# Kernel tuning notes

Hardware: AMD Instinct MI355X
Metric: run time of the kernel (lower is better)

The kernel has to match this reference:

```python
import jax, jax.numpy as jnp
import numpy as np

D_MODEL = 128
D_HIDDEN = 256
D_STATE = 16
EXPAND = 2
D_INNER = EXPAND * D_MODEL  # 256
DT_RANK = (D_MODEL + 15) // 16  # 8, mamba_ssm default ceil(d_model/16)
N = 8192  # decoded reads (sequence length for Mamba)
M = 8192  # encoded reads


def setup_inputs() -> dict:
    key = jax.random.key(0)
    ks = jax.random.split(key, 16)
    s = 0.02
    return {
        "encoded_reads": jax.random.normal(ks[0], (M, D_MODEL), jnp.float32),
        "decoded_reads": jax.random.normal(ks[1], (N, D_MODEL), jnp.float32),
        # Mamba block params (d_conv=1 -> depthwise conv is per-channel affine)
        "in_proj_w": jax.random.normal(ks[2], (2 * D_INNER, D_MODEL), jnp.float32) * s,
        "conv_w": jax.random.normal(ks[3], (D_INNER,), jnp.float32) * s + 1.0,
        "conv_b": jnp.zeros((D_INNER,), jnp.float32),
        "x_proj_w": jax.random.normal(ks[4], (DT_RANK + 2 * D_STATE, D_INNER), jnp.float32) * s,
        "dt_proj_w": jax.random.normal(ks[5], (D_INNER, DT_RANK), jnp.float32) * s,
        "dt_proj_b": jnp.full((D_INNER,), -4.0, jnp.float32),  # softplus(-4)~0.018, typical dt init
        "A_log": jnp.log(jnp.broadcast_to(jnp.arange(1, D_STATE + 1, dtype=jnp.float32), (D_INNER, D_STATE))),
        "D": jnp.ones((D_INNER,), jnp.float32),
        "out_proj_w": jax.random.normal(ks[6], (D_MODEL, D_INNER), jnp.float32) * s,
        # query/key projections (nn.Linear with bias)
        "q_w": jax.random.normal(ks[7], (D_HIDDEN, D_MODEL), jnp.float32) * s,
        "q_b": jnp.zeros((D_HIDDEN,), jnp.float32),
        "k_w": jax.random.normal(ks[8], (D_HIDDEN, D_MODEL), jnp.float32) * s,
        "k_b": jnp.zeros((D_HIDDEN,), jnp.float32),
    }


def _mamba(u, in_proj_w, conv_w, conv_b, x_proj_w, dt_proj_w, dt_proj_b, A_log, D, out_proj_w):
    # u: [L, d_model] treated as a single sequence
    xz = u @ in_proj_w.T                         # [L, 2*d_inner]
    x, z = jnp.split(xz, 2, axis=-1)             # [L, d_inner] each
    # depthwise conv1d with kernel size 1 == per-channel affine, then SiLU
    x = jax.nn.silu(x * conv_w + conv_b)
    x_dbl = x @ x_proj_w.T                       # [L, dt_rank + 2*d_state]
    dt, B, C = jnp.split(x_dbl, [DT_RANK, DT_RANK + D_STATE], axis=-1)
    dt = jax.nn.softplus(dt @ dt_proj_w.T + dt_proj_b)  # [L, d_inner]
    A = -jnp.exp(A_log)                          # [d_inner, d_state]
    deltaA = jnp.exp(dt[:, :, None] * A)         # [L, d_inner, d_state]
    deltaBx = dt[:, :, None] * B[:, None, :] * x[:, :, None]  # [L, d_inner, d_state]

    def step(h, inp):
        dA_t, dBx_t, C_t = inp
        h = dA_t * h + dBx_t                     # [d_inner, d_state]
        y_t = jnp.einsum('dn,n->d', h, C_t)      # [d_inner]
        return h, y_t

    h0 = jnp.zeros((D_INNER, D_STATE), x.dtype)
    _, y = jax.lax.scan(step, h0, (deltaA, deltaBx, C))  # y: [L, d_inner]
    y = (y + D * x) * jax.nn.silu(z)
    return y @ out_proj_w.T                      # [L, d_model]


def reference(encoded_reads, decoded_reads, in_proj_w, conv_w, conv_b, x_proj_w,
              dt_proj_w, dt_proj_b, A_log, D, out_proj_w, q_w, q_b, k_w, k_b):
    decoded_processed = _mamba(decoded_reads, in_proj_w, conv_w, conv_b, x_proj_w,
                               dt_proj_w, dt_proj_b, A_log, D, out_proj_w)
    queries = decoded_processed @ q_w.T + q_b    # [N, d_hidden]
    keys = encoded_reads @ k_w.T + k_b           # [M, d_hidden]
    scores = jnp.einsum('nd,md->nm', queries, keys)
    return jax.nn.softmax(scores, axis=-1)
```

## Files before the change

### kernel.cpp

```cpp
#include <hip/hip_runtime.h>
#include <hip/hip_bf16.h>

typedef __attribute__((ext_vector_type(8))) short bf16x8;
typedef __attribute__((ext_vector_type(4))) float f32x4;

#define LSEQ 8192
#define CHUNK 64
#define NCHUNK 128

__device__ __forceinline__ void gload16(const void* g, void* l) {
    __builtin_amdgcn_global_load_lds(
        (const __attribute__((address_space(1))) void*)g,
        (__attribute__((address_space(3))) void*)l,
        16, 0, 0);
}

__global__ void cvt_bf16_k(const float* __restrict__ src, __hip_bfloat16* __restrict__ dst, int n) {
    int i = blockIdx.x * blockDim.x + threadIdx.x;
    if (i < n) dst[i] = __float2bfloat16(src[i]);
}

template<int OUT_BF16, int HAS_BIAS>
__global__ __launch_bounds__(256) void gemm_bt_k(
    const __hip_bfloat16* __restrict__ A,
    const __hip_bfloat16* __restrict__ B,
    float* __restrict__ Cf, __hip_bfloat16* __restrict__ Cb,
    const float* __restrict__ bias, int M, int N, int K)
{
    __shared__ __hip_bfloat16 As[64][32];
    __shared__ __hip_bfloat16 Bs[64][32];
    const int tid  = threadIdx.x;
    const int wave = tid >> 6;
    const int lane = tid & 63;
    const int wm = (wave >> 1) << 5;
    const int wn = (wave & 1) << 5;
    const long bm = (long)blockIdx.y << 6;
    const long bn = (long)blockIdx.x << 6;

    f32x4 acc[2][2] = {{{0.f,0.f,0.f,0.f},{0.f,0.f,0.f,0.f}},
                       {{0.f,0.f,0.f,0.f},{0.f,0.f,0.f,0.f}}};

    const int sr = tid >> 2;
    const int sc = (tid & 3) << 3;
    const int lr = lane & 15;
    const int kg = (lane >> 4) << 3;

    for (int k0 = 0; k0 < K; k0 += 32) {
        {
            long ar = bm + sr;
            bf16x8 av = {0,0,0,0,0,0,0,0};
            if (ar < M) av = *(const bf16x8*)(A + ar * K + k0 + sc);
            *(bf16x8*)&As[sr][sc] = av;
            long br = bn + sr;
            bf16x8 bv = {0,0,0,0,0,0,0,0};
            if (br < N) bv = *(const bf16x8*)(B + br * K + k0 + sc);
            *(bf16x8*)&Bs[sr][sc] = bv;
        }
        __syncthreads();
        bf16x8 a0 = *(const bf16x8*)&As[wm + lr][kg];
        bf16x8 a1 = *(const bf16x8*)&As[wm + 16 + lr][kg];
        bf16x8 b0 = *(const bf16x8*)&Bs[wn + lr][kg];
        bf16x8 b1 = *(const bf16x8*)&Bs[wn + 16 + lr][kg];
        acc[0][0] = __builtin_amdgcn_mfma_f32_16x16x32_bf16(a0, b0, acc[0][0], 0, 0, 0);
        acc[0][1] = __builtin_amdgcn_mfma_f32_16x16x32_bf16(a0, b1, acc[0][1], 0, 0, 0);
        acc[1][0] = __builtin_amdgcn_mfma_f32_16x16x32_bf16(a1, b0, acc[1][0], 0, 0, 0);
        acc[1][1] = __builtin_amdgcn_mfma_f32_16x16x32_bf16(a1, b1, acc[1][1], 0, 0, 0);
        __syncthreads();
    }
    const int rg = (lane >> 4) << 2;
    #pragma unroll
    for (int i = 0; i < 2; ++i)
      #pragma unroll
      for (int j = 0; j < 2; ++j)
        #pragma unroll
        for (int r = 0; r < 4; ++r) {
            long row = bm + wm + i * 16 + rg + r;
            long col = bn + wn + j * 16 + lr;
            if (row < M && col < N) {
                float v = acc[i][j][r];
                if (HAS_BIAS) v += bias[col];
                if (OUT_BF16) Cb[row * N + col] = __float2bfloat16(v);
                else          Cf[row * N + col] = v;
            }
        }
}

template<int PASS>
__global__ __launch_bounds__(256) void scores_k(
    const __hip_bfloat16* __restrict__ Q, const __hip_bfloat16* __restrict__ Kb,
    float* __restrict__ out, const float* __restrict__ invZ)
{
    __shared__ alignas(16) char Asb[128 * 128];
    __shared__ alignas(16) char Bsb[128 * 128];
    const int tid = threadIdx.x, wave = tid >> 6, lane = tid & 63;
    const int bm = blockIdx.y << 7, bn = blockIdx.x << 7;
    const int wm = (wave >> 1) << 6, wn = (wave & 1) << 6;
    const int K = 256;

    f32x4 acc[4][4];
    #pragma unroll
    for (int i = 0; i < 4; ++i)
      #pragma unroll
      for (int j = 0; j < 4; ++j)
        acc[i][j] = (f32x4){0.f, 0.f, 0.f, 0.f};

    for (int k0 = 0; k0 < 256; k0 += 64) {
        #pragma unroll
        for (int c = 0; c < 4; ++c) {
            const int base = (wave * 4 + c) * 1024;
            const int o = base + lane * 16;
            const int q = o ^ (((o >> 7) & 7) << 4);
            const int row = q >> 7, col = (q & 127) >> 1;
            gload16(Q  + (size_t)(bm + row) * K + k0 + col, Asb + base);
            gload16(Kb + (size_t)(bn + row) * K + k0 + col, Bsb + base);
        }
        __syncthreads();
        #pragma unroll
        for (int ks = 0; ks < 2; ++ks) {
            bf16x8 af[4], bfr[4];
            const int cb = ks * 64 + ((lane >> 4) << 4);
            #pragma unroll
            for (int i = 0; i < 4; ++i) {
                const int ra = wm + i * 16 + (lane & 15);
                af[i]  = *(const bf16x8*)(Asb + ((ra * 128 + cb) ^ ((ra & 7) << 4)));
                const int rb = wn + i * 16 + (lane & 15);
                bfr[i] = *(const bf16x8*)(Bsb + ((rb * 128 + cb) ^ ((rb & 7) << 4)));
            }
            #pragma unroll
            for (int i = 0; i < 4; ++i)
              #pragma unroll
              for (int j = 0; j < 4; ++j)
                acc[i][j] = __builtin_amdgcn_mfma_f32_16x16x32_bf16(af[i], bfr[j], acc[i][j], 0, 0, 0);
        }
        __syncthreads();
    }

    const int lr = lane & 15, rg = (lane >> 4) << 2;
    if (PASS == 0) {
        #pragma unroll
        for (int i = 0; i < 4; ++i) {
            #pragma unroll
            for (int r = 0; r < 4; ++r) {
                float s = __expf(acc[i][0][r]) + __expf(acc[i][1][r])
                        + __expf(acc[i][2][r]) + __expf(acc[i][3][r]);
                #pragma unroll
                for (int o = 1; o < 16; o <<= 1) s += __shfl_xor(s, o, 64);
                if (lr == 0)
                    out[(size_t)(blockIdx.x * 2 + (wave & 1)) * 8192
                        + bm + wm + i * 16 + rg + r] = s;
            }
        }
    } else {
        #pragma unroll
        for (int i = 0; i < 4; ++i)
          #pragma unroll
          for (int r = 0; r < 4; ++r) {
            const int row = bm + wm + i * 16 + rg + r;
            const float iz = invZ[row];
            #pragma unroll
            for (int j = 0; j < 4; ++j)
                out[(size_t)row * 8192 + bn + wn + j * 16 + lr] = __expf(acc[i][j][r]) * iz;
          }
    }
}

__global__ __launch_bounds__(256) void rowsum_inv_k(
    const float* __restrict__ partial, float* __restrict__ invZ)
{
    const int row = blockIdx.x * 256 + threadIdx.x;
    float s = 0.0f;
    for (int c = 0; c < 128; ++c) s += partial[(size_t)c * 8192 + row];
    invZ[row] = 1.0f / s;
}

__global__ __launch_bounds__(256) void conv_silu_k(
    const float* __restrict__ xz, const float* __restrict__ cw, const float* __restrict__ cb,
    float* __restrict__ xf, __hip_bfloat16* __restrict__ xb, float* __restrict__ zs)
{
    const int t = blockIdx.x, d = threadIdx.x;
    float xv = xz[(size_t)t * 512 + d] * cw[d] + cb[d];
    xv = xv / (1.0f + __expf(-xv));
    float zv = xz[(size_t)t * 512 + 256 + d];
    zv = zv / (1.0f + __expf(-zv));
    xf[(size_t)t * 256 + d] = xv;
    xb[(size_t)t * 256 + d] = __float2bfloat16(xv);
    zs[(size_t)t * 256 + d] = zv;
}

__global__ __launch_bounds__(256) void dt_k(
    const float* __restrict__ xdbl, const float* __restrict__ dtw,
    const float* __restrict__ dtb, float* __restrict__ dtv)
{
    __shared__ float r8[8];
    const int t = blockIdx.x, d = threadIdx.x;
    if (d < 8) r8[d] = xdbl[(size_t)t * 40 + d];
    __syncthreads();
    float acc = dtb[d];
    #pragma unroll
    for (int r = 0; r < 8; ++r) acc += r8[r] * dtw[d * 8 + r];
    float sp = (acc > 20.0f) ? acc : logf(1.0f + expf(acc));
    dtv[(size_t)t * 256 + d] = sp;
}

__global__ __launch_bounds__(256) void scan_chunk_k(
    const float* __restrict__ dtv, const float* __restrict__ xf,
    const float* __restrict__ xdbl, const float* __restrict__ A_log,
    float* __restrict__ P, float* __restrict__ S)
{
    __shared__ float Bl[CHUNK * 16];
    const int c = blockIdx.x, d = threadIdx.x;
    const int t0 = c * CHUNK;
    for (int k = d; k < CHUNK * 16; k += 256) {
        int tt = k >> 4, n = k & 15;
        Bl[k] = xdbl[(size_t)(t0 + tt) * 40 + 8 + n];
    }
    __syncthreads();
    float An[16], Pv[16], Sv[16];
    #pragma unroll
    for (int n = 0; n < 16; ++n) { An[n] = -expf(A_log[d * 16 + n]); Pv[n] = 1.0f; Sv[n] = 0.0f; }
    for (int tt = 0; tt < CHUNK; ++tt) {
        float dt = dtv[(size_t)(t0 + tt) * 256 + d];
        float xv = xf[(size_t)(t0 + tt) * 256 + d];
        float dtx = dt * xv;
        #pragma unroll
        for (int n = 0; n < 16; ++n) {
            float a = __expf(dt * An[n]);
            Pv[n] *= a;
            Sv[n] = a * Sv[n] + dtx * Bl[tt * 16 + n];
        }
    }
    size_t base = (size_t)c * 4096 + (size_t)d * 16;
    #pragma unroll
    for (int n = 0; n < 16; ++n) { P[base + n] = Pv[n]; S[base + n] = Sv[n]; }
}

__global__ __launch_bounds__(256) void scan_carry_k(
    const float* __restrict__ P, const float* __restrict__ S, float* __restrict__ hinit)
{
    const int ch = blockIdx.x * 256 + threadIdx.x;
    float h = 0.0f;
    for (int c = 0; c < NCHUNK; ++c) {
        hinit[(size_t)c * 4096 + ch] = h;
        h = P[(size_t)c * 4096 + ch] * h + S[(size_t)c * 4096 + ch];
    }
}

__global__ __launch_bounds__(256) void scan_final_k(
    const float* __restrict__ dtv, const float* __restrict__ xf,
    const float* __restrict__ xdbl, const float* __restrict__ A_log,
    const float* __restrict__ hinit, const float* __restrict__ Dp,
    const float* __restrict__ zs, __hip_bfloat16* __restrict__ yfb)
{
    __shared__ float Bl[CHUNK * 16];
    __shared__ float Cl[CHUNK * 16];
    const int c = blockIdx.x, d = threadIdx.x;
    const int t0 = c * CHUNK;
    for (int k = d; k < CHUNK * 16; k += 256) {
        int tt = k >> 4, n = k & 15;
        Bl[k] = xdbl[(size_t)(t0 + tt) * 40 + 8 + n];
        Cl[k] = xdbl[(size_t)(t0 + tt) * 40 + 24 + n];
    }
    __syncthreads();
    float An[16], h[16];
    #pragma unroll
    for (int n = 0; n < 16; ++n) {
        An[n] = -expf(A_log[d * 16 + n]);
        h[n] = hinit[(size_t)c * 4096 + (size_t)d * 16 + n];
    }
    const float Dv = Dp[d];
    for (int tt = 0; tt < CHUNK; ++tt) {
        float dt = dtv[(size_t)(t0 + tt) * 256 + d];
        float xv = xf[(size_t)(t0 + tt) * 256 + d];
        float dtx = dt * xv;
        float y = 0.0f;
        #pragma unroll
        for (int n = 0; n < 16; ++n) {
            float a = __expf(dt * An[n]);
            h[n] = a * h[n] + dtx * Bl[tt * 16 + n];
            y += h[n] * Cl[tt * 16 + n];
        }
        float outv = (y + Dv * xv) * zs[(size_t)(t0 + tt) * 256 + d];
        yfb[(size_t)(t0 + tt) * 256 + d] = __float2bfloat16(outv);
    }
}

__global__ __launch_bounds__(256) void wc_k(
    const float* __restrict__ qw, const float* __restrict__ opw, __hip_bfloat16* __restrict__ wcb)
{
    const int hh = blockIdx.x, d = threadIdx.x;
    float acc = 0.0f;
    for (int m = 0; m < 128; ++m) acc += qw[hh * 128 + m] * opw[m * 256 + d];
    wcb[hh * 256 + d] = __float2bfloat16(acc);
}

extern "C" void kernel_launch(void* const* d_in, const int* in_sizes, int n_in,
                              void* d_out, int out_size, void* d_ws, size_t ws_size,
                              hipStream_t stream)
{
    const float* enc        = (const float*)d_in[0];
    const float* dec        = (const float*)d_in[1];
    const float* in_proj_w  = (const float*)d_in[2];
    const float* conv_w     = (const float*)d_in[3];
    const float* conv_b     = (const float*)d_in[4];
    const float* x_proj_w   = (const float*)d_in[5];
    const float* dt_proj_w  = (const float*)d_in[6];
    const float* dt_proj_b  = (const float*)d_in[7];
    const float* A_log      = (const float*)d_in[8];
    const float* Dp         = (const float*)d_in[9];
    const float* out_proj_w = (const float*)d_in[10];
    const float* q_w        = (const float*)d_in[11];
    const float* q_b        = (const float*)d_in[12];
    const float* k_w        = (const float*)d_in[13];
    const float* k_b        = (const float*)d_in[14];

    char* ws = (char*)d_ws;
    size_t off = 0;
    auto alloc = [&](size_t bytes) -> void* {
        void* p = ws + off;
        off += (bytes + 255) & ~(size_t)255;
        return p;
    };
    __hip_bfloat16* ub   = (__hip_bfloat16*)alloc((size_t)8192 * 128 * 2);
    __hip_bfloat16* encb = (__hip_bfloat16*)alloc((size_t)8192 * 128 * 2);
    __hip_bfloat16* wib  = (__hip_bfloat16*)alloc((size_t)512 * 128 * 2);
    __hip_bfloat16* wxb  = (__hip_bfloat16*)alloc((size_t)40 * 256 * 2);
    __hip_bfloat16* kwb  = (__hip_bfloat16*)alloc((size_t)256 * 128 * 2);
    __hip_bfloat16* wcb  = (__hip_bfloat16*)alloc((size_t)256 * 256 * 2);
    float* xz    = (float*)alloc((size_t)8192 * 512 * 4);
    float* xf    = (float*)alloc((size_t)8192 * 256 * 4);
    __hip_bfloat16* xb = (__hip_bfloat16*)alloc((size_t)8192 * 256 * 2);
    float* zs    = (float*)alloc((size_t)8192 * 256 * 4);
    float* xdbl  = (float*)alloc((size_t)8192 * 40 * 4);
    float* dtv   = (float*)alloc((size_t)8192 * 256 * 4);
    float* P     = (float*)alloc((size_t)NCHUNK * 4096 * 4);
    float* Ssum  = (float*)alloc((size_t)NCHUNK * 4096 * 4);
    float* hinit = (float*)alloc((size_t)NCHUNK * 4096 * 4);
    __hip_bfloat16* yfb = (__hip_bfloat16*)alloc((size_t)8192 * 256 * 2);
    __hip_bfloat16* qbm = (__hip_bfloat16*)alloc((size_t)8192 * 256 * 2);
    __hip_bfloat16* kbm = (__hip_bfloat16*)alloc((size_t)8192 * 256 * 2);
    float* partial = (float*)alloc((size_t)128 * 8192 * 4);
    float* invZ    = (float*)alloc((size_t)8192 * 4);
    (void)ws_size;

    cvt_bf16_k<<<(8192 * 128 + 255) / 256, 256, 0, stream>>>(dec, ub, 8192 * 128);
    cvt_bf16_k<<<(8192 * 128 + 255) / 256, 256, 0, stream>>>(enc, encb, 8192 * 128);
    cvt_bf16_k<<<(512 * 128 + 255) / 256, 256, 0, stream>>>(in_proj_w, wib, 512 * 128);
    cvt_bf16_k<<<(40 * 256 + 255) / 256, 256, 0, stream>>>(x_proj_w, wxb, 40 * 256);
    cvt_bf16_k<<<(256 * 128 + 255) / 256, 256, 0, stream>>>(k_w, kwb, 256 * 128);

    {
        dim3 g(512 / 64, 8192 / 64);
        gemm_bt_k<0, 0><<<g, 256, 0, stream>>>(ub, wib, xz, nullptr, nullptr, 8192, 512, 128);
    }
    conv_silu_k<<<8192, 256, 0, stream>>>(xz, conv_w, conv_b, xf, xb, zs);

    {
        dim3 g(1, 8192 / 64);
        gemm_bt_k<0, 0><<<g, 256, 0, stream>>>(xb, wxb, xdbl, nullptr, nullptr, 8192, 40, 256);
    }
    dt_k<<<8192, 256, 0, stream>>>(xdbl, dt_proj_w, dt_proj_b, dtv);

    scan_chunk_k<<<NCHUNK, 256, 0, stream>>>(dtv, xf, xdbl, A_log, P, Ssum);
    scan_carry_k<<<16, 256, 0, stream>>>(P, Ssum, hinit);
    scan_final_k<<<NCHUNK, 256, 0, stream>>>(dtv, xf, xdbl, A_log, hinit, Dp, zs, yfb);

    wc_k<<<256, 256, 0, stream>>>(q_w, out_proj_w, wcb);

    {
        dim3 g(256 / 64, 8192 / 64);
        gemm_bt_k<1, 1><<<g, 256, 0, stream>>>(yfb, wcb, nullptr, qbm, q_b, 8192, 256, 256);
    }
    {
        dim3 g(256 / 64, 8192 / 64);
        gemm_bt_k<1, 1><<<g, 256, 0, stream>>>(encb, kwb, nullptr, kbm, k_b, 8192, 256, 128);
    }

    {
        dim3 g(8192 / 128, 8192 / 128);
        scores_k<0><<<g, 256, 0, stream>>>(qbm, kbm, partial, nullptr);
        rowsum_inv_k<<<8192 / 256, 256, 0, stream>>>(partial, invZ);
        scores_k<1><<<g, 256, 0, stream>>>(qbm, kbm, (float*)d_out, invZ);
    }
}
```

Baseline: 287.7 us.

## Fuse conversions, conv/SiLU and dt projection into GEMMs and scan kernels

Merges all weight conversions and the out_proj·q_w weight fold into one prep kernel, and makes the in_proj and key GEMMs read fp32 activations directly, converting them to bf16 while loading into LDS. The conv+SiLU epilogue moves into the in_proj GEMM, and the dt projection with its softplus is recomputed inside both scan kernels from xdbl kept in LDS. The scan chunk size is halved to 32 so twice as many blocks run, and the LDS rows are padded to 40 to reduce bank conflicts. This removes several launches and the xz, dtv and bf16 input round-trips through memory, at the cost of computing softplus twice and a longer carry-scan loop.

```diff
diff --git a/kernel.cpp b/kernel.cpp
--- a/kernel.cpp
+++ b/kernel.cpp
@@ -4,9 +4,8 @@
 typedef __attribute__((ext_vector_type(8))) short bf16x8;
 typedef __attribute__((ext_vector_type(4))) float f32x4;
 
-#define LSEQ 8192
-#define CHUNK 64
-#define NCHUNK 128
+#define CHUNK 32
+#define NCHUNK 256
 
 __device__ __forceinline__ void gload16(const void* g, void* l) {
     __builtin_amdgcn_global_load_lds(
@@ -15,9 +14,27 @@
         16, 0, 0);
 }
 
-__global__ void cvt_bf16_k(const float* __restrict__ src, __hip_bfloat16* __restrict__ dst, int n) {
-    int i = blockIdx.x * blockDim.x + threadIdx.x;
-    if (i < n) dst[i] = __float2bfloat16(src[i]);
+__device__ __forceinline__ float silu_f(float v) { return v / (1.0f + __expf(-v)); }
+
+__global__ __launch_bounds__(256) void prep_k(
+    const float* __restrict__ in_proj_w, const float* __restrict__ x_proj_w,
+    const float* __restrict__ k_w, const float* __restrict__ q_w,
+    const float* __restrict__ out_proj_w,
+    __hip_bfloat16* __restrict__ wib, __hip_bfloat16* __restrict__ wxb,
+    __hip_bfloat16* __restrict__ kwb, __hip_bfloat16* __restrict__ wcb)
+{
+    const int b = blockIdx.x, t = threadIdx.x;
+    if (b < 424) {
+        int idx = b * 256 + t;
+        if (idx < 65536)      wib[idx]         = __float2bfloat16(in_proj_w[idx]);
+        else if (idx < 75776) wxb[idx - 65536] = __float2bfloat16(x_proj_w[idx - 65536]);
+        else                  kwb[idx - 75776] = __float2bfloat16(k_w[idx - 75776]);
+    } else {
+        const int hh = b - 424;
+        float acc = 0.0f;
+        for (int m = 0; m < 128; ++m) acc += q_w[hh * 128 + m] * out_proj_w[m * 256 + t];
+        wcb[hh * 256 + t] = __float2bfloat16(acc);
+    }
 }
 
 template<int OUT_BF16, int HAS_BIAS>
@@ -27,8 +44,8 @@
     float* __restrict__ Cf, __hip_bfloat16* __restrict__ Cb,
     const float* __restrict__ bias, int M, int N, int K)
 {
-    __shared__ __hip_bfloat16 As[64][32];
-    __shared__ __hip_bfloat16 Bs[64][32];
+    __shared__ __hip_bfloat16 As[64][40];
+    __shared__ __hip_bfloat16 Bs[64][40];
     const int tid  = threadIdx.x;
     const int wave = tid >> 6;
     const int lane = tid & 63;
@@ -81,6 +98,83 @@
                 if (HAS_BIAS) v += bias[col];
                 if (OUT_BF16) Cb[row * N + col] = __float2bfloat16(v);
                 else          Cf[row * N + col] = v;
+            }
+        }
+}
+
+template<int EPI>
+__global__ __launch_bounds__(256) void gemm_f32a_k(
+    const float* __restrict__ A, const __hip_bfloat16* __restrict__ B,
+    const float* __restrict__ w0, const float* __restrict__ w1,
+    float* __restrict__ xf, __hip_bfloat16* __restrict__ ob, float* __restrict__ zs,
+    int M, int N, int K)
+{
+    __shared__ __hip_bfloat16 As[64][40];
+    __shared__ __hip_bfloat16 Bs[64][40];
+    const int tid  = threadIdx.x;
+    const int wave = tid >> 6;
+    const int lane = tid & 63;
+    const int wm = (wave >> 1) << 5;
+    const int wn = (wave & 1) << 5;
+    const long bm = (long)blockIdx.y << 6;
+    const long bn = (long)blockIdx.x << 6;
+
+    f32x4 acc[2][2] = {{{0.f,0.f,0.f,0.f},{0.f,0.f,0.f,0.f}},
+                       {{0.f,0.f,0.f,0.f},{0.f,0.f,0.f,0.f}}};
+
+    const int sr = tid >> 2;
+    const int sc = (tid & 3) << 3;
+    const int lr = lane & 15;
+    const int kg = (lane >> 4) << 3;
+
+    for (int k0 = 0; k0 < K; k0 += 32) {
+        {
+            long ar = bm + sr;
+            f32x4 x0 = *(const f32x4*)(A + ar * K + k0 + sc);
+            f32x4 x1 = *(const f32x4*)(A + ar * K + k0 + sc + 4);
+            union { bf16x8 v; __hip_bfloat16 h[8]; } u;
+            u.h[0] = __float2bfloat16(x0[0]); u.h[1] = __float2bfloat16(x0[1]);
+            u.h[2] = __float2bfloat16(x0[2]); u.h[3] = __float2bfloat16(x0[3]);
+            u.h[4] = __float2bfloat16(x1[0]); u.h[5] = __float2bfloat16(x1[1]);
+            u.h[6] = __float2bfloat16(x1[2]); u.h[7] = __float2bfloat16(x1[3]);
+            *(bf16x8*)&As[sr][sc] = u.v;
+            long br = bn + sr;
+            bf16x8 bv = {0,0,0,0,0,0,0,0};
+            if (br < N) bv = *(const bf16x8*)(B + br * K + k0 + sc);
+            *(bf16x8*)&Bs[sr][sc] = bv;
+        }
+        __syncthreads();
+        bf16x8 a0 = *(const bf16x8*)&As[wm + lr][kg];
+        bf16x8 a1 = *(const bf16x8*)&As[wm + 16 + lr][kg];
+        bf16x8 b0 = *(const bf16x8*)&Bs[wn + lr][kg];
+        bf16x8 b1 = *(const bf16x8*)&Bs[wn + 16 + lr][kg];
+        acc[0][0] = __builtin_amdgcn_mfma_f32_16x16x32_bf16(a0, b0, acc[0][0], 0, 0, 0);
+        acc[0][1] = __builtin_amdgcn_mfma_f32_16x16x32_bf16(a0, b1, acc[0][1], 0, 0, 0);
+        acc[1][0] = __builtin_amdgcn_mfma_f32_16x16x32_bf16(a1, b0, acc[1][0], 0, 0, 0);
+        acc[1][1] = __builtin_amdgcn_mfma_f32_16x16x32_bf16(a1, b1, acc[1][1], 0, 0, 0);
+        __syncthreads();
+    }
+    const int rg = (lane >> 4) << 2;
+    #pragma unroll
+    for (int i = 0; i < 2; ++i)
+      #pragma unroll
+      for (int j = 0; j < 2; ++j)
+        #pragma unroll
+        for (int r = 0; r < 4; ++r) {
+            long row = bm + wm + i * 16 + rg + r;
+            long col = bn + wn + j * 16 + lr;
+            float v = acc[i][j][r];
+            if (EPI == 0) {
+                if (col < 256) {
+                    float xv = v * w0[col] + w1[col];
+                    float s = silu_f(xv);
+                    xf[row * 256 + col] = s;
+                    ob[row * 256 + col] = __float2bfloat16(s);
+                } else {
+                    zs[row * 256 + col - 256] = silu_f(v);
+                }
+            } else {
+                ob[row * N + col] = __float2bfloat16(v + w0[col]);
             }
         }
 }
@@ -173,60 +267,35 @@
     invZ[row] = 1.0f / s;
 }
 
-__global__ __launch_bounds__(256) void conv_silu_k(
-    const float* __restrict__ xz, const float* __restrict__ cw, const float* __restrict__ cb,
-    float* __restrict__ xf, __hip_bfloat16* __restrict__ xb, float* __restrict__ zs)
-{
-    const int t = blockIdx.x, d = threadIdx.x;
-    float xv = xz[(size_t)t * 512 + d] * cw[d] + cb[d];
-    xv = xv / (1.0f + __expf(-xv));
-    float zv = xz[(size_t)t * 512 + 256 + d];
-    zv = zv / (1.0f + __expf(-zv));
-    xf[(size_t)t * 256 + d] = xv;
-    xb[(size_t)t * 256 + d] = __float2bfloat16(xv);
-    zs[(size_t)t * 256 + d] = zv;
-}
-
-__global__ __launch_bounds__(256) void dt_k(
-    const float* __restrict__ xdbl, const float* __restrict__ dtw,
-    const float* __restrict__ dtb, float* __restrict__ dtv)
-{
-    __shared__ float r8[8];
-    const int t = blockIdx.x, d = threadIdx.x;
-    if (d < 8) r8[d] = xdbl[(size_t)t * 40 + d];
-    __syncthreads();
-    float acc = dtb[d];
-    #pragma unroll
-    for (int r = 0; r < 8; ++r) acc += r8[r] * dtw[d * 8 + r];
-    float sp = (acc > 20.0f) ? acc : logf(1.0f + expf(acc));
-    dtv[(size_t)t * 256 + d] = sp;
-}
-
 __global__ __launch_bounds__(256) void scan_chunk_k(
-    const float* __restrict__ dtv, const float* __restrict__ xf,
-    const float* __restrict__ xdbl, const float* __restrict__ A_log,
+    const float* __restrict__ xf, const float* __restrict__ xdbl,
+    const float* __restrict__ dtw, const float* __restrict__ dtb,
+    const float* __restrict__ A_log,
     float* __restrict__ P, float* __restrict__ S)
 {
-    __shared__ float Bl[CHUNK * 16];
+    __shared__ float xs[CHUNK * 40];
     const int c = blockIdx.x, d = threadIdx.x;
     const int t0 = c * CHUNK;
-    for (int k = d; k < CHUNK * 16; k += 256) {
-        int tt = k >> 4, n = k & 15;
-        Bl[k] = xdbl[(size_t)(t0 + tt) * 40 + 8 + n];
-    }
+    for (int k = d; k < CHUNK * 40; k += 256) xs[k] = xdbl[(size_t)t0 * 40 + k];
     __syncthreads();
+    const f32x4 wa = *(const f32x4*)(dtw + d * 8);
+    const f32x4 wb = *(const f32x4*)(dtw + d * 8 + 4);
+    const float dbias = dtb[d];
     float An[16], Pv[16], Sv[16];
     #pragma unroll
     for (int n = 0; n < 16; ++n) { An[n] = -expf(A_log[d * 16 + n]); Pv[n] = 1.0f; Sv[n] = 0.0f; }
     for (int tt = 0; tt < CHUNK; ++tt) {
-        float dt = dtv[(size_t)(t0 + tt) * 256 + d];
+        const float* xr = xs + tt * 40;
+        float dr = dbias + xr[0]*wa[0] + xr[1]*wa[1] + xr[2]*wa[2] + xr[3]*wa[3]
+                         + xr[4]*wb[0] + xr[5]*wb[1] + xr[6]*wb[2] + xr[7]*wb[3];
+        float dt = (dr > 20.0f) ? dr : logf(1.0f + expf(dr));
         float xv = xf[(size_t)(t0 + tt) * 256 + d];
         float dtx = dt * xv;
         #pragma unroll
         for (int n = 0; n < 16; ++n) {
             float a = __expf(dt * An[n]);
             Pv[n] *= a;
-            Sv[n] = a * Sv[n] + dtx * Bl[tt * 16 + n];
+            Sv[n] = a * Sv[n] + dtx * xr[8 + n];
         }
     }
     size_t base = (size_t)c * 4096 + (size_t)d * 16;
@@ -246,21 +315,20 @@
 }
 
 __global__ __launch_bounds__(256) void scan_final_k(
-    const float* __restrict__ dtv, const float* __restrict__ xf,
-    const float* __restrict__ xdbl, const float* __restrict__ A_log,
-    const float* __restrict__ hinit, const float* __restrict__ Dp,
-    const float* __restrict__ zs, __hip_bfloat16* __restrict__ yfb)
-{
-    __shared__ float Bl[CHUNK * 16];
-    __shared__ float Cl[CHUNK * 16];
+    const float* __restrict__ xf, const float* __restrict__ xdbl,
+    const float* __restrict__ dtw, const float* __restrict__ dtb,
+    const float* __restrict__ A_log, const float* __restrict__ hinit,
+    const float* __restrict__ Dp, const float* __restrict__ zs,
+    __hip_bfloat16* __restrict__ yfb)
+{
+    __shared__ float xs[CHUNK * 40];
     const int c = blockIdx.x, d = threadIdx.x;
     const int t0 = c * CHUNK;
-    for (int k = d; k < CHUNK * 16; k += 256) {
-        int tt = k >> 4, n = k & 15;
-        Bl[k] = xdbl[(size_t)(t0 + tt) * 40 + 8 + n];
-        Cl[k] = xdbl[(size_t)(t0 + tt) * 40 + 24 + n];
-    }
+    for (int k = d; k < CHUNK * 40; k += 256) xs[k] = xdbl[(size_t)t0 * 40 + k];
     __syncthreads();
+    const f32x4 wa = *(const f32x4*)(dtw + d * 8);
+    const f32x4 wb = *(const f32x4*)(dtw + d * 8 + 4);
+    const float dbias = dtb[d];
     float An[16], h[16];
     #pragma unroll
     for (int n = 0; n < 16; ++n) {
@@ -269,28 +337,22 @@
     }
     const float Dv = Dp[d];
     for (int tt = 0; tt < CHUNK; ++tt) {
-        float dt = dtv[(size_t)(t0 + tt) * 256 + d];
+        const float* xr = xs + tt * 40;
+        float dr = dbias + xr[0]*wa[0] + xr[1]*wa[1] + xr[2]*wa[2] + xr[3]*wa[3]
+                         + xr[4]*wb[0] + xr[5]*wb[1] + xr[6]*wb[2] + xr[7]*wb[3];
+        float dt = (dr > 20.0f) ? dr : logf(1.0f + expf(dr));
         float xv = xf[(size_t)(t0 + tt) * 256 + d];
         float dtx = dt * xv;
         float y = 0.0f;
         #pragma unroll
         for (int n = 0; n < 16; ++n) {
             float a = __expf(dt * An[n]);
-            h[n] = a * h[n] + dtx * Bl[tt * 16 + n];
-            y += h[n] * Cl[tt * 16 + n];
+            h[n] = a * h[n] + dtx * xr[8 + n];
+            y += h[n] * xr[24 + n];
         }
         float outv = (y + Dv * xv) * zs[(size_t)(t0 + tt) * 256 + d];
         yfb[(size_t)(t0 + tt) * 256 + d] = __float2bfloat16(outv);
     }
-}
-
-__global__ __launch_bounds__(256) void wc_k(
-    const float* __restrict__ qw, const float* __restrict__ opw, __hip_bfloat16* __restrict__ wcb)
-{
-    const int hh = blockIdx.x, d = threadIdx.x;
-    float acc = 0.0f;
-    for (int m = 0; m < 128; ++m) acc += qw[hh * 128 + m] * opw[m * 256 + d];
-    wcb[hh * 256 + d] = __float2bfloat16(acc);
 }
 
 extern "C" void kernel_launch(void* const* d_in, const int* in_sizes, int n_in,
@@ -320,18 +382,14 @@
         off += (bytes + 255) & ~(size_t)255;
         return p;
     };
-    __hip_bfloat16* ub   = (__hip_bfloat16*)alloc((size_t)8192 * 128 * 2);
-    __hip_bfloat16* encb = (__hip_bfloat16*)alloc((size_t)8192 * 128 * 2);
     __hip_bfloat16* wib  = (__hip_bfloat16*)alloc((size_t)512 * 128 * 2);
     __hip_bfloat16* wxb  = (__hip_bfloat16*)alloc((size_t)40 * 256 * 2);
     __hip_bfloat16* kwb  = (__hip_bfloat16*)alloc((size_t)256 * 128 * 2);
     __hip_bfloat16* wcb  = (__hip_bfloat16*)alloc((size_t)256 * 256 * 2);
-    float* xz    = (float*)alloc((size_t)8192 * 512 * 4);
     float* xf    = (float*)alloc((size_t)8192 * 256 * 4);
     __hip_bfloat16* xb = (__hip_bfloat16*)alloc((size_t)8192 * 256 * 2);
     float* zs    = (float*)alloc((size_t)8192 * 256 * 4);
     float* xdbl  = (float*)alloc((size_t)8192 * 40 * 4);
-    float* dtv   = (float*)alloc((size_t)8192 * 256 * 4);
     float* P     = (float*)alloc((size_t)NCHUNK * 4096 * 4);
     float* Ssum  = (float*)alloc((size_t)NCHUNK * 4096 * 4);
     float* hinit = (float*)alloc((size_t)NCHUNK * 4096 * 4);
@@ -342,29 +400,22 @@
     float* invZ    = (float*)alloc((size_t)8192 * 4);
     (void)ws_size;
 
-    cvt_bf16_k<<<(8192 * 128 + 255) / 256, 256, 0, stream>>>(dec, ub, 8192 * 128);
-    cvt_bf16_k<<<(8192 * 128 + 255) / 256, 256, 0, stream>>>(enc, encb, 8192 * 128);
-    cvt_bf16_k<<<(512 * 128 + 255) / 256, 256, 0, stream>>>(in_proj_w, wib, 512 * 128);
-    cvt_bf16_k<<<(40 * 256 + 255) / 256, 256, 0, stream>>>(x_proj_w, wxb, 40 * 256);
-    cvt_bf16_k<<<(256 * 128 + 255) / 256, 256, 0, stream>>>(k_w, kwb, 256 * 128);
+    prep_k<<<680, 256, 0, stream>>>(in_proj_w, x_proj_w, k_w, q_w, out_proj_w,
+                                    wib, wxb, kwb, wcb);
 
     {
         dim3 g(512 / 64, 8192 / 64);
-        gemm_bt_k<0, 0><<<g, 256, 0, stream>>>(ub, wib, xz, nullptr, nullptr, 8192, 512, 128);
-    }
-    conv_silu_k<<<8192, 256, 0, stream>>>(xz, conv_w, conv_b, xf, xb, zs);
-
+        gemm_f32a_k<0><<<g, 256, 0, stream>>>(dec, wib, conv_w, conv_b,
+                                              xf, xb, zs, 8192, 512, 128);
+    }
     {
         dim3 g(1, 8192 / 64);
         gemm_bt_k<0, 0><<<g, 256, 0, stream>>>(xb, wxb, xdbl, nullptr, nullptr, 8192, 40, 256);
     }
-    dt_k<<<8192, 256, 0, stream>>>(xdbl, dt_proj_w, dt_proj_b, dtv);
-
-    scan_chunk_k<<<NCHUNK, 256, 0, stream>>>(dtv, xf, xdbl, A_log, P, Ssum);
+    scan_chunk_k<<<NCHUNK, 256, 0, stream>>>(xf, xdbl, dt_proj_w, dt_proj_b, A_log, P, Ssum);
     scan_carry_k<<<16, 256, 0, stream>>>(P, Ssum, hinit);
-    scan_final_k<<<NCHUNK, 256, 0, stream>>>(dtv, xf, xdbl, A_log, hinit, Dp, zs, yfb);
-
-    wc_k<<<256, 256, 0, stream>>>(q_w, out_proj_w, wcb);
+    scan_final_k<<<NCHUNK, 256, 0, stream>>>(xf, xdbl, dt_proj_w, dt_proj_b, A_log,
+                                             hinit, Dp, zs, yfb);
 
     {
         dim3 g(256 / 64, 8192 / 64);
@@ -372,7 +423,8 @@
     }
     {
         dim3 g(256 / 64, 8192 / 64);
-        gemm_bt_k<1, 1><<<g, 256, 0, stream>>>(encb, kwb, nullptr, kbm, k_b, 8192, 256, 128);
+        gemm_f32a_k<1><<<g, 256, 0, stream>>>(enc, kwb, k_b, nullptr,
+                                              nullptr, kbm, nullptr, 8192, 256, 128);
     }
 
     {
```

After: 239.9 us. -16.6%, faster.
